# Performance work log

Measured on AMD Instinct MI355X. Metric: run time of the kernel, lower is better.

## Reference

```python
import jax, jax.numpy as jnp
import numpy as np

BLOCK_SIZE = 1024
OUTLIER_SIGMA = 3.0
OUT_FEATURES = 11008
IN_FEATURES = 4096
TOKENS = 64


def _quantize_mixed_np(W):
    """Faithful numpy port of quantize_mixed (BLOCK_SIZE divides numel exactly here)."""
    flat = W.astype(np.float32).reshape(-1)
    nb = flat.size // BLOCK_SIZE
    blocks = flat.reshape(nb, BLOCK_SIZE)
    mu = blocks.mean(axis=1, keepdims=True)
    sig = np.maximum(blocks.std(axis=1, ddof=1, keepdims=True), 1e-8)  # torch.std is unbiased
    outlier = np.abs(blocks - mu) > OUTLIER_SIGMA * sig
    abs_max = np.maximum(np.abs(np.where(outlier, 0.0, blocks)).max(axis=1), 1e-8)
    scales = (abs_max / 127.0).astype(np.float16)
    q = np.clip(np.round(blocks / abs_max[:, None] * 127.0), -127, 127).astype(np.int8)
    all_pos = np.arange(nb, dtype=np.int64)[:, None] * BLOCK_SIZE + np.arange(BLOCK_SIZE, dtype=np.int64)[None, :]
    int8_data = q[~outlier]                      # row-major == torch order
    fp16_data = blocks[outlier].astype(np.float16)
    int8_pos = all_pos[~outlier].astype(np.int32)
    fp16_pos = all_pos[outlier].astype(np.int32)
    block_idx = np.nonzero(~outlier)[0].astype(np.int32)  # block index per int8 value
    return int8_data, fp16_data, scales, int8_pos, fp16_pos, block_idx


def setup_inputs() -> dict:
    key = jax.random.key(0)
    k_x, k_b = jax.random.split(key)
    rng = np.random.default_rng(0)
    W = (rng.standard_normal((OUT_FEATURES, IN_FEATURES)) * 0.02).astype(np.float32)
    int8_data, fp16_data, scales, int8_pos, fp16_pos, block_idx = _quantize_mixed_np(W)
    x = jax.random.normal(k_x, (TOKENS, IN_FEATURES), dtype=jnp.float16)
    bias = jax.random.normal(k_b, (OUT_FEATURES,), dtype=jnp.float16) * jnp.float16(0.02)
    return {
        "x": x,
        "int8_data": jnp.asarray(int8_data),
        "fp16_data": jnp.asarray(fp16_data),
        "scales": jnp.asarray(scales),
        "bias": bias,
        "int8_pos": jnp.asarray(int8_pos),
        "fp16_pos": jnp.asarray(fp16_pos),
        "block_idx": jnp.asarray(block_idx),
    }


def reference(x, int8_data, fp16_data, scales, bias, int8_pos, fp16_pos, block_idx):
    out_features = bias.shape[0]
    in_features = x.shape[1]
    numel = out_features * in_features  # divisible by BLOCK_SIZE for these dims
    # dequantize_mixed: scatter fp16 outliers and dequantized int8 values into flat fp16 buffer
    flat = jnp.zeros((numel,), dtype=jnp.float16)
    flat = flat.at[fp16_pos].set(fp16_data)
    flat = flat.at[int8_pos].set(int8_data.astype(jnp.float16) * scales[block_idx])
    W = flat.reshape(out_features, in_features)
    # F.linear(x, W, bias) in fp16
    return jnp.dot(x.astype(jnp.float16), W.T) + bias
```

## Files before the change

kernel.cpp:

```cpp
#include <hip/hip_runtime.h>
#include <hip/hip_fp16.h>

#define TOK   64
#define INF   4096
#define OUTF  11008
#define NUMEL (OUTF * INF)
#define NSLC  (NUMEL / 64)
#define NBLK  (OUTF / 16)
#define KSPL  4
#define OUTN  (TOK * OUTF)

typedef __attribute__((ext_vector_type(8))) _Float16 half8;
typedef __attribute__((ext_vector_type(4))) _Float16 half4;
typedef __attribute__((ext_vector_type(4))) float floatx4;
typedef __attribute__((ext_vector_type(4), aligned(4))) int int4u;
typedef __attribute__((ext_vector_type(4))) int int4a;

#define TPAD 72

__global__ __launch_bounds__(256) void precompute_kernel(
    const float* __restrict__ x, const int* __restrict__ fppos, int nf,
    _Float16* __restrict__ x16, int* __restrict__ meta) {
  const int t = blockIdx.x * 256 + threadIdx.x;
  if (t < (TOK * INF) / 4) {
    const floatx4 f = *(const floatx4*)&x[t * 4];
    half4 h;
    h[0] = (_Float16)f[0]; h[1] = (_Float16)f[1];
    h[2] = (_Float16)f[2]; h[3] = (_Float16)f[3];
    *(half4*)&x16[t * 4] = h;
  }
  if (t < NSLC) {
    const int target = t << 6;
    int lo = 0, hi = nf;
    while (lo < hi) {
      const int mid = (lo + hi) >> 1;
      if (fppos[mid] < target) lo = mid + 1; else hi = mid;
    }
    unsigned long long mask = 0ull;
    int j = lo;
    while (j < nf) {
      const int d = fppos[j] - target;
      if (d >= 64) break;
      mask |= 1ull << d;
      ++j;
    }
    int4a mv;
    mv[0] = lo;
    mv[1] = (int)(unsigned)(mask & 0xffffffffu);
    mv[2] = (int)(unsigned)(mask >> 32);
    mv[3] = 0;
    *(int4a*)&meta[t * 4] = mv;
  }
}

__device__ __forceinline__ void window16(const int p0, const int4a mv,
                                         int& i0a, unsigned& m8a,
                                         int& i0b, unsigned& m8b) {
  const unsigned mlo = (unsigned)mv[1];
  const unsigned mhi = (unsigned)mv[2];
  const int off = p0 & 63;
  const unsigned w32 = (off & 32) ? mhi : mlo;
  const unsigned m16 = (off & 16) ? (w32 >> 16) : (w32 & 0xffffu);
  int ltb = 0;
  if (off & 32) ltb += __popc(mlo);
  if (off & 16) ltb += __popc(w32 & 0xffffu);
  m8a = m16 & 0xffu;
  m8b = (m16 >> 8) & 0xffu;
  i0a = p0 - mv[0] - ltb;
  i0b = i0a + 8 - __popc(m8a);
}

__device__ __forceinline__ half8 finish_slot(
    const unsigned m8, const int i0, const int p0, const float s,
    const int (&l)[8], const int* __restrict__ i8,
    const float* __restrict__ fpdat, const int n8) {
  const int f = (int)m8;
  float ov[8];
#pragma unroll
  for (int e = 0; e < 8; ++e) ov[e] = 0.f;
  if (f) {
    int fi = p0 - i0;
#pragma unroll
    for (int e = 0; e < 8; ++e) {
      if ((f >> e) & 1) { ov[e] = fpdat[fi]; ++fi; }
    }
  }

  half8 oh;
  if (i0 + 8 <= n8) {
    if (f == 0) {
#pragma unroll
      for (int e = 0; e < 8; ++e) oh[e] = (_Float16)((float)l[e] * s);
    } else {
      int q = 0;
#pragma unroll
      for (int e = 0; e < 8; ++e) {
        const int flg = (f >> e) & 1;
        int lv = l[0];
#pragma unroll
        for (int qq = 1; qq < 8; ++qq) lv = (q == qq) ? l[qq] : lv;
        oh[e] = flg ? (_Float16)ov[e] : (_Float16)((float)lv * s);
        q += 1 - flg;
      }
    }
  } else {
    int c = 0;
    const int m = n8 - 1;
#pragma unroll
    for (int e = 0; e < 8; ++e) {
      const int flg = (f >> e) & 1;
      int idx = i0 + e - c;
      idx = idx < 0 ? 0 : (idx > m ? m : idx);
      oh[e] = flg ? (_Float16)ov[e] : (_Float16)((float)i8[idx] * s);
      c += flg;
    }
  }
  return oh;
}

struct Bank {
  int la[8];
  int lb[8];
  int i0a, i0b;
  unsigned m8a, m8b;
};

__global__ __launch_bounds__(256, 4) void gemm_fused(
    const _Float16* __restrict__ x16, const int* __restrict__ i8,
    const float* __restrict__ fpdat, const float* __restrict__ scales,
    const int* __restrict__ meta, float* __restrict__ part, const int n8) {
  __shared__ __attribute__((aligned(16))) char smem[4 * 2 * 16 * TPAD * 2];
  _Float16 (* __restrict__ tiles)[2][16][TPAD] = (_Float16 (*)[2][16][TPAD])smem;
  float* red = (float*)smem;

  const int tid  = threadIdx.x;
  const int wave = tid >> 6;
  const int lane = tid & 63;
  const int nt   = blockIdx.x >> 2;
  const int kq   = blockIdx.x & 3;
  const int n0   = nt << 4;
  const int kbas = kq * 1024 + wave * 256;

  const int srow  = lane >> 2;
  const int ssub  = lane & 3;
  const int prow  = n0 + srow;
  const int pbase = prow * INF + kbas;
  const float s   = scales[prow * 4 + kq];

  const int ln   = lane & 15;
  const int quad = lane >> 4;

#define ISSUE(BNK, P0, MV)                                          \
  do {                                                              \
    window16((P0), (MV), BNK.i0a, BNK.m8a, BNK.i0b, BNK.m8b);       \
    if (BNK.i0a + 8 <= n8) {                                        \
      *(int4u*)&BNK.la[0] = *(const int4u*)&i8[BNK.i0a];            \
      *(int4u*)&BNK.la[4] = *(const int4u*)&i8[BNK.i0a + 4];        \
    }                                                               \
    if (BNK.i0b + 8 <= n8) {                                        \
      *(int4u*)&BNK.lb[0] = *(const int4u*)&i8[BNK.i0b];            \
      *(int4u*)&BNK.lb[4] = *(const int4u*)&i8[BNK.i0b + 4];        \
    }                                                               \
  } while (0)

#define FINISH(BNK, P0, LB)                                                  \
  do {                                                                       \
    const half8 ha_ = finish_slot(BNK.m8a, BNK.i0a, (P0), s, BNK.la,         \
                                  i8, fpdat, n8);                            \
    const half8 hb_ = finish_slot(BNK.m8b, BNK.i0b, (P0) + 8, s, BNK.lb,     \
                                  i8, fpdat, n8);                            \
    *(half8*)&tiles[wave][LB][srow][ssub * 16]     = ha_;                    \
    *(half8*)&tiles[wave][LB][srow][ssub * 16 + 8] = hb_;                    \
  } while (0)

#define MFMA_STEP(CC, LB)                                                    \
  do {                                                                       \
    const _Float16* ap_ = &x16[ln * INF + kbas + (CC) * 64 + quad * 8];      \
    const _Float16* bp_ = &tiles[wave][LB][ln][quad * 8];                    \
    _Pragma("unroll")                                                        \
    for (int st = 0; st < 2; ++st) {                                         \
      const int ko = st * 32;                                                \
      const half8 bh = *(const half8*)&bp_[ko];                              \
      const half8 a0 = *(const half8*)&ap_[ko];                              \
      const half8 a1 = *(const half8*)&ap_[16 * INF + ko];                   \
      const half8 a2 = *(const half8*)&ap_[32 * INF + ko];                   \
      const half8 a3 = *(const half8*)&ap_[48 * INF + ko];                   \
      acc0 = __builtin_amdgcn_mfma_f32_16x16x32_f16(a0, bh, acc0, 0, 0, 0);  \
      acc1 = __builtin_amdgcn_mfma_f32_16x16x32_f16(a1, bh, acc1, 0, 0, 0);  \
      acc2 = __builtin_amdgcn_mfma_f32_16x16x32_f16(a2, bh, acc2, 0, 0, 0);  \
      acc3 = __builtin_amdgcn_mfma_f32_16x16x32_f16(a3, bh, acc3, 0, 0, 0);  \
    }                                                                        \
  } while (0)

  int4a mz0 = *(const int4a*)&meta[(pbase >> 6) * 4];
  int4a mz1 = *(const int4a*)&meta[((pbase + 64) >> 6) * 4];
  Bank bA, bB;
  ISSUE(bA, pbase + ssub * 16, mz0);

  floatx4 acc0 = {0,0,0,0}, acc1 = {0,0,0,0}, acc2 = {0,0,0,0}, acc3 = {0,0,0,0};

  ISSUE(bB, pbase + 64 + ssub * 16, mz1);
  mz0 = *(const int4a*)&meta[((pbase + 128) >> 6) * 4];
  FINISH(bA, pbase + ssub * 16, 0);
  MFMA_STEP(0, 0);
  ISSUE(bA, pbase + 128 + ssub * 16, mz0);
  mz1 = *(const int4a*)&meta[((pbase + 192) >> 6) * 4];
  FINISH(bB, pbase + 64 + ssub * 16, 1);
  MFMA_STEP(1, 1);
  ISSUE(bB, pbase + 192 + ssub * 16, mz1);
  FINISH(bA, pbase + 128 + ssub * 16, 0);
  MFMA_STEP(2, 0);
  FINISH(bB, pbase + 192 + ssub * 16, 1);
  MFMA_STEP(3, 1);

#undef ISSUE
#undef FINISH
#undef MFMA_STEP

  __syncthreads();

  const int mb = quad * 4;
#pragma unroll
  for (int i = 0; i < 4; ++i) red[wave * 1024 + (mb + i)      * 16 + ln] = acc0[i];
#pragma unroll
  for (int i = 0; i < 4; ++i) red[wave * 1024 + (16 + mb + i) * 16 + ln] = acc1[i];
#pragma unroll
  for (int i = 0; i < 4; ++i) red[wave * 1024 + (32 + mb + i) * 16 + ln] = acc2[i];
#pragma unroll
  for (int i = 0; i < 4; ++i) red[wave * 1024 + (48 + mb + i) * 16 + ln] = acc3[i];
  __syncthreads();

  float* pp = &part[(size_t)kq * OUTN];
#pragma unroll
  for (int c2 = 0; c2 < 4; ++c2) {
    const int cell = tid + c2 * 256;
    const int mm = cell >> 4, nn = cell & 15;
    pp[mm * OUTF + n0 + nn] =
        red[cell] + red[1024 + cell] + red[2048 + cell] + red[3072 + cell];
  }
}

__global__ __launch_bounds__(256) void reduce_kernel(
    const float* __restrict__ part, const float* __restrict__ bias,
    float* __restrict__ out) {
  const int t  = blockIdx.x * 256 + threadIdx.x;
  const int i4 = t * 4;
  floatx4 a = *(const floatx4*)&part[i4];
#pragma unroll
  for (int k = 1; k < KSPL; ++k) {
    const floatx4 b = *(const floatx4*)&part[(size_t)k * OUTN + i4];
    a[0] += b[0]; a[1] += b[1]; a[2] += b[2]; a[3] += b[3];
  }
  const int nn = i4 % OUTF;
  const floatx4 bb = *(const floatx4*)&bias[nn];
  a[0] += bb[0]; a[1] += bb[1]; a[2] += bb[2]; a[3] += bb[3];
  *(floatx4*)&out[i4] = a;
}

extern "C" void kernel_launch(void* const* d_in, const int* in_sizes, int n_in,
                              void* d_out, int out_size, void* d_ws,
                              size_t ws_size, hipStream_t stream) {
  const float* x      = (const float*)d_in[0];
  const int*   i8     = (const int*)d_in[1];
  const float* fpdat  = (const float*)d_in[2];
  const float* scales = (const float*)d_in[3];
  const float* bias   = (const float*)d_in[4];
  const int*   fppos  = (const int*)d_in[6];

  char* wsp = (char*)d_ws;
  _Float16* x16  = (_Float16*)wsp;
  int*      meta = (int*)(wsp + (size_t)TOK * INF * sizeof(_Float16));
  float*    part = (float*)(wsp + (size_t)TOK * INF * sizeof(_Float16)
                                + (size_t)NSLC * 16);
  float*    out  = (float*)d_out;

  const int n8 = in_sizes[1];
  const int nf = in_sizes[2];

  precompute_kernel<<<NSLC / 256, 256, 0, stream>>>(x, fppos, nf, x16, meta);
  gemm_fused<<<NBLK * KSPL, 256, 0, stream>>>(x16, i8, fpdat, scales, meta,
                                              part, n8);
  reduce_kernel<<<OUTN / (4 * 256), 256, 0, stream>>>(part, bias, out);
}
```

Baseline: 450.8 us.

## Dequantize weights directly into MFMA B-operand registers, bypassing LDS staging

Each lane now dequantizes the exact 8-element K slices it feeds to the MFMA B operand, so the LDS tile write, read and the barrier before the reduction are removed. Activation A fragments and up to two outlier values per slot are prefetched into registers during the issue phase, and the slow general path runs only when a wave holds a slot with more than two outliers. This raises register pressure, so the occupancy hint drops from 4 to 3 blocks per CU, and the per-element select chains add VALU work.

```diff
diff --git a/kernel.cpp b/kernel.cpp
--- a/kernel.cpp
+++ b/kernel.cpp
@@ -15,8 +15,6 @@
 typedef __attribute__((ext_vector_type(4))) float floatx4;
 typedef __attribute__((ext_vector_type(4), aligned(4))) int int4u;
 typedef __attribute__((ext_vector_type(4))) int int4a;
-
-#define TPAD 72
 
 __global__ __launch_bounds__(256) void precompute_kernel(
     const float* __restrict__ x, const int* __restrict__ fppos, int nf,
@@ -53,21 +51,15 @@
   }
 }
 
-__device__ __forceinline__ void window16(const int p0, const int4a mv,
-                                         int& i0a, unsigned& m8a,
-                                         int& i0b, unsigned& m8b) {
+__device__ __forceinline__ void meta_window1(const int p0, const int4a mv,
+                                             int& i0, unsigned& m8) {
   const unsigned mlo = (unsigned)mv[1];
   const unsigned mhi = (unsigned)mv[2];
   const int off = p0 & 63;
-  const unsigned w32 = (off & 32) ? mhi : mlo;
-  const unsigned m16 = (off & 16) ? (w32 >> 16) : (w32 & 0xffffu);
-  int ltb = 0;
-  if (off & 32) ltb += __popc(mlo);
-  if (off & 16) ltb += __popc(w32 & 0xffffu);
-  m8a = m16 & 0xffu;
-  m8b = (m16 >> 8) & 0xffu;
-  i0a = p0 - mv[0] - ltb;
-  i0b = i0a + 8 - __popc(m8a);
+  m8 = 0xffu & (off < 32 ? (mlo >> off) : (mhi >> (off - 32)));
+  const unsigned bl = (off >= 32) ? mlo : (mlo & ((1u << off) - 1u));
+  const unsigned bh = (off >= 32) ? (mhi & ((1u << (off - 32)) - 1u)) : 0u;
+  i0 = p0 - mv[0] - (__popc(bl) + __popc(bh));
 }
 
 __device__ __forceinline__ half8 finish_slot(
@@ -118,106 +110,150 @@
   return oh;
 }
 
-struct Bank {
-  int la[8];
-  int lb[8];
+struct Pre {
+  int la[8], lb[8];
   int i0a, i0b;
   unsigned m8a, m8b;
+  float va0, va1, vb0, vb1;
+  half8 A[8];
 };
 
-__global__ __launch_bounds__(256, 4) void gemm_fused(
+__global__ __launch_bounds__(256, 3) void gemm_fused(
     const _Float16* __restrict__ x16, const int* __restrict__ i8,
     const float* __restrict__ fpdat, const float* __restrict__ scales,
-    const int* __restrict__ meta, float* __restrict__ part, const int n8) {
-  __shared__ __attribute__((aligned(16))) char smem[4 * 2 * 16 * TPAD * 2];
-  _Float16 (* __restrict__ tiles)[2][16][TPAD] = (_Float16 (*)[2][16][TPAD])smem;
-  float* red = (float*)smem;
+    const int* __restrict__ meta, float* __restrict__ part,
+    const int n8, const int nf) {
+  __shared__ float red[4 * 64 * 16];
 
   const int tid  = threadIdx.x;
   const int wave = tid >> 6;
   const int lane = tid & 63;
+  const int quad = lane >> 4;
+  const int ln   = lane & 15;
   const int nt   = blockIdx.x >> 2;
   const int kq   = blockIdx.x & 3;
   const int n0   = nt << 4;
   const int kbas = kq * 1024 + wave * 256;
-
-  const int srow  = lane >> 2;
-  const int ssub  = lane & 3;
-  const int prow  = n0 + srow;
+  const int qoff = quad * 8;
+
+  const int prow  = n0 + ln;
   const int pbase = prow * INF + kbas;
   const float s   = scales[prow * 4 + kq];
 
-  const int ln   = lane & 15;
-  const int quad = lane >> 4;
-
-#define ISSUE(BNK, P0, MV)                                          \
-  do {                                                              \
-    window16((P0), (MV), BNK.i0a, BNK.m8a, BNK.i0b, BNK.m8b);       \
-    if (BNK.i0a + 8 <= n8) {                                        \
-      *(int4u*)&BNK.la[0] = *(const int4u*)&i8[BNK.i0a];            \
-      *(int4u*)&BNK.la[4] = *(const int4u*)&i8[BNK.i0a + 4];        \
-    }                                                               \
-    if (BNK.i0b + 8 <= n8) {                                        \
-      *(int4u*)&BNK.lb[0] = *(const int4u*)&i8[BNK.i0b];            \
-      *(int4u*)&BNK.lb[4] = *(const int4u*)&i8[BNK.i0b + 4];        \
-    }                                                               \
+#define ISSUE(BNK, CC, MV)                                                   \
+  do {                                                                       \
+    const int p0a_ = pbase + (CC) * 64 + qoff;                               \
+    meta_window1(p0a_, (MV), BNK.i0a, BNK.m8a);                              \
+    meta_window1(p0a_ + 32, (MV), BNK.i0b, BNK.m8b);                         \
+    if (BNK.i0a + 8 <= n8) {                                                 \
+      *(int4u*)&BNK.la[0] = *(const int4u*)&i8[BNK.i0a];                     \
+      *(int4u*)&BNK.la[4] = *(const int4u*)&i8[BNK.i0a + 4];                 \
+    }                                                                        \
+    if (BNK.i0b + 8 <= n8) {                                                 \
+      *(int4u*)&BNK.lb[0] = *(const int4u*)&i8[BNK.i0b];                     \
+      *(int4u*)&BNK.lb[4] = *(const int4u*)&i8[BNK.i0b + 4];                 \
+    }                                                                        \
+    if (BNK.m8a) {                                                           \
+      const int fia_ = p0a_ - BNK.i0a;                                       \
+      BNK.va0 = fpdat[fia_];                                                 \
+      BNK.va1 = fpdat[fia_ + 1 < nf ? fia_ + 1 : nf - 1];                    \
+    }                                                                        \
+    if (BNK.m8b) {                                                           \
+      const int fib_ = p0a_ + 32 - BNK.i0b;                                  \
+      BNK.vb0 = fpdat[fib_];                                                 \
+      BNK.vb1 = fpdat[fib_ + 1 < nf ? fib_ + 1 : nf - 1];                    \
+    }                                                                        \
+    const _Float16* ap_ = &x16[ln * INF + kbas + (CC) * 64 + qoff];          \
+    BNK.A[0] = *(const half8*)&ap_[0];                                       \
+    BNK.A[1] = *(const half8*)&ap_[16 * INF];                                \
+    BNK.A[2] = *(const half8*)&ap_[32 * INF];                                \
+    BNK.A[3] = *(const half8*)&ap_[48 * INF];                                \
+    BNK.A[4] = *(const half8*)&ap_[32];                                      \
+    BNK.A[5] = *(const half8*)&ap_[16 * INF + 32];                           \
+    BNK.A[6] = *(const half8*)&ap_[32 * INF + 32];                           \
+    BNK.A[7] = *(const half8*)&ap_[48 * INF + 32];                           \
   } while (0)
 
-#define FINISH(BNK, P0, LB)                                                  \
+#define FSLOT(OH, LARR, M8, I0, V0, V1)                                      \
   do {                                                                       \
-    const half8 ha_ = finish_slot(BNK.m8a, BNK.i0a, (P0), s, BNK.la,         \
-                                  i8, fpdat, n8);                            \
-    const half8 hb_ = finish_slot(BNK.m8b, BNK.i0b, (P0) + 8, s, BNK.lb,     \
-                                  i8, fpdat, n8);                            \
-    *(half8*)&tiles[wave][LB][srow][ssub * 16]     = ha_;                    \
-    *(half8*)&tiles[wave][LB][srow][ssub * 16 + 8] = hb_;                    \
+    const int f_ = (int)(M8);                                                \
+    if ((I0) + 8 <= n8) {                                                    \
+      if (f_ == 0) {                                                         \
+        _Pragma("unroll")                                                    \
+        for (int e = 0; e < 8; ++e) OH[e] = (_Float16)((float)LARR[e] * s);  \
+      } else {                                                               \
+        int q_ = 0;                                                          \
+        _Pragma("unroll")                                                    \
+        for (int e = 0; e < 8; ++e) {                                        \
+          const int flg = (f_ >> e) & 1;                                     \
+          const int rank = __popc(f_ & ((1 << e) - 1));                      \
+          const float fv = (rank == 0) ? (V0) : (V1);                        \
+          int lv = LARR[0];                                                  \
+          _Pragma("unroll")                                                  \
+          for (int qq = 1; qq < 8; ++qq) lv = (q_ == qq) ? LARR[qq] : lv;    \
+          OH[e] = flg ? (_Float16)fv : (_Float16)((float)lv * s);            \
+          q_ += 1 - flg;                                                     \
+        }                                                                    \
+      }                                                                      \
+    } else {                                                                 \
+      int c_ = 0;                                                            \
+      const int m_ = n8 - 1;                                                 \
+      _Pragma("unroll")                                                      \
+      for (int e = 0; e < 8; ++e) {                                          \
+        const int flg = (f_ >> e) & 1;                                       \
+        const int rank = __popc(f_ & ((1 << e) - 1));                        \
+        const float fv = (rank == 0) ? (V0) : (V1);                          \
+        int idx = (I0) + e - c_;                                             \
+        idx = idx < 0 ? 0 : (idx > m_ ? m_ : idx);                           \
+        OH[e] = flg ? (_Float16)fv : (_Float16)((float)i8[idx] * s);         \
+        c_ += flg;                                                           \
+      }                                                                      \
+    }                                                                        \
   } while (0)
 
-#define MFMA_STEP(CC, LB)                                                    \
+#define FIN_MFMA(BNK, CC)                                                    \
   do {                                                                       \
-    const _Float16* ap_ = &x16[ln * INF + kbas + (CC) * 64 + quad * 8];      \
-    const _Float16* bp_ = &tiles[wave][LB][ln][quad * 8];                    \
-    _Pragma("unroll")                                                        \
-    for (int st = 0; st < 2; ++st) {                                         \
-      const int ko = st * 32;                                                \
-      const half8 bh = *(const half8*)&bp_[ko];                              \
-      const half8 a0 = *(const half8*)&ap_[ko];                              \
-      const half8 a1 = *(const half8*)&ap_[16 * INF + ko];                   \
-      const half8 a2 = *(const half8*)&ap_[32 * INF + ko];                   \
-      const half8 a3 = *(const half8*)&ap_[48 * INF + ko];                   \
-      acc0 = __builtin_amdgcn_mfma_f32_16x16x32_f16(a0, bh, acc0, 0, 0, 0);  \
-      acc1 = __builtin_amdgcn_mfma_f32_16x16x32_f16(a1, bh, acc1, 0, 0, 0);  \
-      acc2 = __builtin_amdgcn_mfma_f32_16x16x32_f16(a2, bh, acc2, 0, 0, 0);  \
-      acc3 = __builtin_amdgcn_mfma_f32_16x16x32_f16(a3, bh, acc3, 0, 0, 0);  \
-    }                                                                        \
+    const int p0a_ = pbase + (CC) * 64 + qoff;                               \
+    half8 b0, b1;                                                            \
+    FSLOT(b0, BNK.la, BNK.m8a, BNK.i0a, BNK.va0, BNK.va1);                   \
+    FSLOT(b1, BNK.lb, BNK.m8b, BNK.i0b, BNK.vb0, BNK.vb1);                   \
+    if (__any(__popc((int)BNK.m8a) > 2 || __popc((int)BNK.m8b) > 2)) {       \
+      if (__popc((int)BNK.m8a) > 2)                                          \
+        b0 = finish_slot(BNK.m8a, BNK.i0a, p0a_, s, BNK.la, i8, fpdat, n8);  \
+      if (__popc((int)BNK.m8b) > 2)                                          \
+        b1 = finish_slot(BNK.m8b, BNK.i0b, p0a_ + 32, s, BNK.lb,             \
+                         i8, fpdat, n8);                                     \
+    }                                                                        \
+    acc0 = __builtin_amdgcn_mfma_f32_16x16x32_f16(BNK.A[0], b0, acc0, 0,0,0);\
+    acc1 = __builtin_amdgcn_mfma_f32_16x16x32_f16(BNK.A[1], b0, acc1, 0,0,0);\
+    acc2 = __builtin_amdgcn_mfma_f32_16x16x32_f16(BNK.A[2], b0, acc2, 0,0,0);\
+    acc3 = __builtin_amdgcn_mfma_f32_16x16x32_f16(BNK.A[3], b0, acc3, 0,0,0);\
+    acc0 = __builtin_amdgcn_mfma_f32_16x16x32_f16(BNK.A[4], b1, acc0, 0,0,0);\
+    acc1 = __builtin_amdgcn_mfma_f32_16x16x32_f16(BNK.A[5], b1, acc1, 0,0,0);\
+    acc2 = __builtin_amdgcn_mfma_f32_16x16x32_f16(BNK.A[6], b1, acc2, 0,0,0);\
+    acc3 = __builtin_amdgcn_mfma_f32_16x16x32_f16(BNK.A[7], b1, acc3, 0,0,0);\
   } while (0)
 
-  int4a mz0 = *(const int4a*)&meta[(pbase >> 6) * 4];
-  int4a mz1 = *(const int4a*)&meta[((pbase + 64) >> 6) * 4];
-  Bank bA, bB;
-  ISSUE(bA, pbase + ssub * 16, mz0);
+  int4a mzA = *(const int4a*)&meta[(pbase >> 6) * 4];
+  int4a mzB = *(const int4a*)&meta[((pbase + 64) >> 6) * 4];
+  Pre pA, pB;
+  ISSUE(pA, 0, mzA);
 
   floatx4 acc0 = {0,0,0,0}, acc1 = {0,0,0,0}, acc2 = {0,0,0,0}, acc3 = {0,0,0,0};
 
-  ISSUE(bB, pbase + 64 + ssub * 16, mz1);
-  mz0 = *(const int4a*)&meta[((pbase + 128) >> 6) * 4];
-  FINISH(bA, pbase + ssub * 16, 0);
-  MFMA_STEP(0, 0);
-  ISSUE(bA, pbase + 128 + ssub * 16, mz0);
-  mz1 = *(const int4a*)&meta[((pbase + 192) >> 6) * 4];
-  FINISH(bB, pbase + 64 + ssub * 16, 1);
-  MFMA_STEP(1, 1);
-  ISSUE(bB, pbase + 192 + ssub * 16, mz1);
-  FINISH(bA, pbase + 128 + ssub * 16, 0);
-  MFMA_STEP(2, 0);
-  FINISH(bB, pbase + 192 + ssub * 16, 1);
-  MFMA_STEP(3, 1);
+  ISSUE(pB, 1, mzB);
+  mzA = *(const int4a*)&meta[((pbase + 128) >> 6) * 4];
+  FIN_MFMA(pA, 0);
+  ISSUE(pA, 2, mzA);
+  mzB = *(const int4a*)&meta[((pbase + 192) >> 6) * 4];
+  FIN_MFMA(pB, 1);
+  ISSUE(pB, 3, mzB);
+  FIN_MFMA(pA, 2);
+  FIN_MFMA(pB, 3);
 
 #undef ISSUE
-#undef FINISH
-#undef MFMA_STEP
-
-  __syncthreads();
+#undef FSLOT
+#undef FIN_MFMA
 
   const int mb = quad * 4;
 #pragma unroll
@@ -279,6 +315,6 @@
 
   precompute_kernel<<<NSLC / 256, 256, 0, stream>>>(x, fppos, nf, x16, meta);
   gemm_fused<<<NBLK * KSPL, 256, 0, stream>>>(x16, i8, fpdat, scales, meta,
-                                              part, n8);
+                                              part, n8, nf);
   reduce_kernel<<<OUTN / (4 * 256), 256, 0, stream>>>(part, bias, out);
 }
```

New measurement: 438.3 us. -2.8%, faster.
